# Performance work log

Measured on AMD Instinct MI355X. Metric: run time of the kernel, lower is better.

## Reference

```python
import jax, jax.numpy as jnp
import numpy as np

N, T, H, D = 512, 256, 512, 9  # batch, decode steps, hidden, feature dim


def setup_inputs() -> dict:
    key = jax.random.key(0)
    ks = jax.random.split(key, 4)
    s = 1.0 / np.sqrt(H)
    return {
        "x": jax.random.normal(ks[0], (N, T + 1, D), dtype=jnp.float32),
        "W_ih": jax.random.normal(ks[1], (4 * H, D), dtype=jnp.float32) * s,
        "W_hh": jax.random.normal(ks[2], (4 * H, H), dtype=jnp.float32) * s,
        "b_ih": jnp.zeros((4 * H,), dtype=jnp.float32),
        "b_hh": jnp.zeros((4 * H,), dtype=jnp.float32),
        "fc_W": jax.random.normal(ks[3], (D, H), dtype=jnp.float32) * s,
        "fc_b": jnp.zeros((D,), dtype=jnp.float32),
        "h0": jnp.zeros((1, H), dtype=jnp.float32),
        "c0": jnp.zeros((1, H), dtype=jnp.float32),
    }


def _lstm_cell(x_proj, h, c, W_hh, b_hh):
    # x_proj = x @ W_ih.T + b_ih, precomputed. PyTorch LSTMCell gate order: i, f, g, o
    gates = x_proj + h @ W_hh.T + b_hh
    i, f, g, o = jnp.split(gates, 4, axis=-1)
    c_new = jax.nn.sigmoid(f) * c + jax.nn.sigmoid(i) * jnp.tanh(g)
    h_new = jax.nn.sigmoid(o) * jnp.tanh(c_new)
    return h_new, c_new


def reference(x, W_ih, W_hh, b_ih, b_hh, fc_W, fc_b, h0, c0):
    n = x.shape[0]
    h = jnp.broadcast_to(h0, (n, h0.shape[1]))
    c = jnp.broadcast_to(c0, (n, c0.shape[1]))

    # Encode phase: consume all T+1 input steps (precompute input projections in one GEMM)
    x_proj = jnp.einsum('ntd,gd->tng', x, W_ih) + b_ih  # [T+1, N, 4H]

    def enc_step(carry, xp):
        h, c = carry
        h, c = _lstm_cell(xp, h, c, W_hh, b_hh)
        return (h, c), None

    (h, c), _ = jax.lax.scan(enc_step, (h, c), x_proj)

    # Decode phase: T steps with zero input (input projection reduces to b_ih)
    zero_proj = jnp.broadcast_to(b_ih, (n, b_ih.shape[0]))

    def dec_step(carry, _):
        h, c = carry
        h, c = _lstm_cell(zero_proj, h, c, W_hh, b_hh)
        out = jax.nn.sigmoid(h @ fc_W.T + fc_b)  # [N, D]
        return (h, c), out

    n_dec = x.shape[1] - 1
    _, outs = jax.lax.scan(dec_step, (h, c), None, length=n_dec)  # [T, N, D]
    return jnp.transpose(outs, (1, 0, 2))  # [N, T, D]
```

## Files before the change

kernel.cpp:

```cpp
#include <hip/hip_runtime.h>


#define TT 256
#define HH 512
#define DD 9
#define TP1 257
#define NSTEP 513
#define THREADS 512
#define NWG 256
#define NCL 8
#define WPC 32

#define WF_HI_B 0u
#define WF_LO_B 2097152u
#define HFRAG_B 4194304u
#define U32_B   8388608u

#define L_ST    0
#define L_EX    16384
#define L_HNEW  20480
#define L_WIH   21520
#define L_MISC  22160
#define L_TOT   22164

typedef short s8v __attribute__((ext_vector_type(8)));
typedef float f4v __attribute__((ext_vector_type(4)));
typedef int   i4v __attribute__((ext_vector_type(4)));

__device__ __forceinline__ float sigmoidf_(float v){ return 1.0f/(1.0f+__expf(-v)); }
__device__ __forceinline__ float tanhf_(float v){ return 1.0f - 2.0f/(__expf(2.0f*v)+1.0f); }
__device__ __forceinline__ unsigned short bf16hi_rne(float f){
    unsigned u = __float_as_uint(f);
    return (unsigned short)((u + 0x7fffu + ((u>>16)&1u)) >> 16);
}
#define B2F_LO(u) __uint_as_float(((unsigned)(u))<<16)
#define B2F_HI(u) __uint_as_float(((unsigned)(u)) & 0xffff0000u)

__device__ __forceinline__ void ld16i(i4v& d, const char* p){
    asm volatile("global_load_dwordx4 %0, %1, off sc0" : "=v"(d) : "v"(p));
}
__device__ __forceinline__ void wait_vm0_mem(){
    asm volatile("s_waitcnt vmcnt(0)" ::: "memory");
}
__device__ __forceinline__ void wait_vm0_4i(i4v& a0,i4v& a1,i4v& a2,i4v& a3){
    asm volatile("s_waitcnt vmcnt(0)"
                 : "+v"(a0),"+v"(a1),"+v"(a2),"+v"(a3) :: "memory");
}
__device__ __forceinline__ void lgkm0_bar(){
    asm volatile("s_waitcnt lgkmcnt(0)" ::: "memory");
    __builtin_amdgcn_s_barrier();
}

__global__ void rnn_init_kernel(const float* __restrict__ W_hh,
                                const float* __restrict__ h0,
                                char* __restrict__ wsb) {
    int idx = blockIdx.x * blockDim.x + threadIdx.x;
    {
        int i  = idx & 7;
        int l  = (idx >> 3) & 63;
        int kt = (idx >> 9) & 15;
        int rb = (idx >> 13) & 3;
        int wl = idx >> 15;
        int mm = l & 15, gg = l >> 4;
        int gt = mm & 3, lu = mm >> 2;
        int grow = gt * 512 + wl * 16 + rb * 4 + lu;
        int k = kt * 32 + gg * 8 + i;
        float v = W_hh[grow * 512 + k];
        unsigned short hi = bf16hi_rne(v);
        float fh = __uint_as_float(((unsigned)hi) << 16);
        unsigned short lo = bf16hi_rne(v - fh);
        ((unsigned short*)(wsb + WF_HI_B))[idx] = hi;
        ((unsigned short*)(wsb + WF_LO_B))[idx] = lo;
    }
    if (idx < 262144) {
        int i   = idx & 7;
        int gg  = (idx >> 9) & 3;
        int kt  = (idx >> 11) & 15;
        int cl  = idx >> 15;
        int rem = idx & 32767;
        int j = kt * 32 + gg * 8 + i;
        ((unsigned short*)(wsb + HFRAG_B + (unsigned)cl * 65536u))[rem] = bf16hi_rne(h0[j]);
    }
    if (idx < 2048) ((unsigned int*)(wsb + U32_B))[idx] = 0u;
}

__global__ __attribute__((amdgpu_waves_per_eu(2, 2))) __launch_bounds__(THREADS)
void rnn_persist_kernel(const float* __restrict__ x,
                        const float* __restrict__ W_ih,
                        const float* __restrict__ b_ih,
                        const float* __restrict__ b_hh,
                        const float* __restrict__ fc_W,
                        const float* __restrict__ fc_b,
                        const float* __restrict__ c0,
                        char* __restrict__ wsb,
                        float* __restrict__ out) {
    __shared__ float smem[L_TOT];
    char* ldsst = (char*)smem;

    const int wg  = blockIdx.x;
    const int cl  = wg & 7;
    const int wl  = wg >> 3;
    const int nb0 = cl * 64;
    const int tid = threadIdx.x;
    const int lane = tid & 63;
    const int wid  = tid >> 6;
    const int rb   = wid & 3;
    const int kh   = wid >> 2;
    const int m    = lane & 15;
    const int g    = lane >> 4;
    const int gu   = wl * 16 + rb * 4 + g;
    const int c0i  = kh * 32 + m;

    unsigned int* flags = (unsigned int*)(wsb + U32_B);
    unsigned int* ctr   = (unsigned int*)(wsb + U32_B + 3072);
    unsigned int* xccb  = (unsigned int*)(wsb + U32_B + 4096);

    for (int i2 = tid; i2 < 16 * 36; i2 += THREADS) {
        int u = i2 / 36; int r2 = i2 - u * 36; int gt = r2 / 9; int d = r2 - gt * 9;
        smem[L_WIH + u * 40 + gt * 9 + d] = W_ih[(gt * 512 + wl * 16 + u) * DD + d];
    }

    const float bias0 = b_ih[gu]        + b_hh[gu];
    const float bias1 = b_ih[512 + gu]  + b_hh[512 + gu];
    const float bias2 = b_ih[1024 + gu] + b_hh[1024 + gu];
    const float bias3 = b_ih[1536 + gu] + b_hh[1536 + gu];
    float creg0 = c0[gu], creg1 = c0[gu];

    s8v wAh[8], wAl[8];
    {
        const char* base = wsb + (unsigned)(((wl*4 + rb)*16 + kh*8)*64 + lane)*16u;
#pragma unroll
        for (int j = 0; j < 8; ++j) {
            wAh[j] = *(const s8v*)(base + WF_HI_B + j*1024);
            wAl[j] = *(const s8v*)(base + WF_LO_B + j*1024);
        }
    }

    if (tid == 0) {
        unsigned xcc;
        asm volatile("s_getreg_b32 %0, hwreg(HW_REG_XCC_ID, 0, 32)" : "=s"(xcc));
        __hip_atomic_store(xccb + wg, xcc + 1u, __ATOMIC_RELAXED, __HIP_MEMORY_SCOPE_AGENT);
        __hip_atomic_fetch_add(ctr, 1u, __ATOMIC_RELEASE, __HIP_MEMORY_SCOPE_AGENT);
        while (__hip_atomic_load(ctr, __ATOMIC_RELAXED, __HIP_MEMORY_SCOPE_AGENT) < NWG)
            __builtin_amdgcn_s_sleep(8);
    }
    __syncthreads();
    {
        unsigned v = (tid < WPC)
            ? __hip_atomic_load(xccb + cl + 8 * tid, __ATOMIC_RELAXED,
                                __HIP_MEMORY_SCOPE_AGENT) : 0u;
        unsigned v0 = __shfl(v, 0, 64);
        bool ok = (tid >= WPC) || (v != 0u && v == v0);
        unsigned long long mk = __ballot(ok);
        if (tid == 0) smem[L_MISC] = (mk == ~0ull) ? 1.0f : 0.0f;
    }
    __syncthreads();
    const bool fast = (smem[L_MISC] != 0.0f);

    const int fg = tid >> 4, fl = tid & 15;

    for (int s = 0; s < NSTEP; ++s) {
        const int par = s & 1;
        const char* hsrc = wsb + HFRAG_B + (unsigned)(par*8 + cl) * 65536u;
        unsigned int* flg = flags + cl * 32;
        const bool dec = (s >= TP1 + 1);
        const bool enc = (s < TP1);

        float xv0[DD], xv1[DD];
        if (enc) {
            const float* xp0 = x + (size_t)(nb0 + c0i) * (TP1 * DD) + s * DD;
            const float* xp1 = x + (size_t)(nb0 + c0i + 16) * (TP1 * DD) + s * DD;
#pragma unroll
            for (int d = 0; d < DD; ++d) { xv0[d] = xp0[d]; xv1[d] = xp1[d]; }
        }

        if (s > 0) {
            if (tid < WPC) {
                for (;;) {
                    unsigned v = __hip_atomic_load(flg + tid, __ATOMIC_RELAXED,
                                                   __HIP_MEMORY_SCOPE_AGENT);
                    if (__all((int)(v >= (unsigned)s))) break;
                    __builtin_amdgcn_s_sleep(2);
                }
            }
            __syncthreads();
            if (fast) __builtin_amdgcn_fence(__ATOMIC_ACQUIRE, "workgroup");
            else      __builtin_amdgcn_fence(__ATOMIC_ACQUIRE, "agent");
        }

        i4v hb[8];
#pragma unroll
        for (int c = 0; c < 8; ++c)
            ld16i(hb[c], hsrc + c*8192 + tid*16);

        wait_vm0_mem();
#pragma unroll
        for (int c = 0; c < 8; ++c)
            *(i4v*)(ldsst + c*8192 + tid*16) = hb[c];
        i4v qa0, qa1, qa2, qa3;
        if (dec) {
            const int bselL = (fg < 2 * DD) ? (fg / DD) : 0;
            const int blL = wl * 2 + bselL;
            const char* hp = hsrc + fl*4096 + blL*16;
            ld16i(qa0, hp);          ld16i(qa1, hp + 1024);
            ld16i(qa2, hp + 2048);   ld16i(qa3, hp + 3072);
        }
        lgkm0_bar();

        f4v a0 = {0,0,0,0}, a1 = {0,0,0,0}, a2 = {0,0,0,0}, a3 = {0,0,0,0};
        {
            const char* base = ldsst + kh*32768;
#pragma unroll
            for (int j = 0; j < 8; ++j) {
                const char* bb = base + j*4096 + g*1024 + m*16;
                s8v bh0 = *(const s8v*)(bb);
                s8v bh1 = *(const s8v*)(bb + 256);
                s8v bh2 = *(const s8v*)(bb + 512);
                s8v bh3 = *(const s8v*)(bb + 768);
                a0 = __builtin_amdgcn_mfma_f32_16x16x32_bf16(wAh[j], bh0, a0, 0,0,0);
                a1 = __builtin_amdgcn_mfma_f32_16x16x32_bf16(wAh[j], bh1, a1, 0,0,0);
                a2 = __builtin_amdgcn_mfma_f32_16x16x32_bf16(wAh[j], bh2, a2, 0,0,0);
                a3 = __builtin_amdgcn_mfma_f32_16x16x32_bf16(wAh[j], bh3, a3, 0,0,0);
                a0 = __builtin_amdgcn_mfma_f32_16x16x32_bf16(wAl[j], bh0, a0, 0,0,0);
                a1 = __builtin_amdgcn_mfma_f32_16x16x32_bf16(wAl[j], bh1, a1, 0,0,0);
                a2 = __builtin_amdgcn_mfma_f32_16x16x32_bf16(wAl[j], bh2, a2, 0,0,0);
                a3 = __builtin_amdgcn_mfma_f32_16x16x32_bf16(wAl[j], bh3, a3, 0,0,0);
            }
            float* pe = smem + L_EX + ((rb*2 + kh)*64 + lane)*8;
            if (kh == 0) { *(f4v*)(pe) = a2; *(f4v*)(pe + 4) = a3; }
            else         { *(f4v*)(pe) = a0; *(f4v*)(pe + 4) = a1; }
        }
        lgkm0_bar();

        {
            const float* px = smem + L_EX + ((rb*2 + (kh^1))*64 + lane)*8;
            f4v r0 = *(const f4v*)(px);
            f4v r1 = *(const f4v*)(px + 4);
            f4v ka, kb;
            if (kh == 0) { ka = a0 + r0; kb = a1 + r1; }
            else         { ka = a2 + r0; kb = a3 + r1; }

            float s00=0,s01=0,s02=0,s03=0, s10=0,s11=0,s12=0,s13=0;
            if (enc) {
                const float* wb2 = smem + L_WIH + (rb*4 + g) * 40;
#pragma unroll
                for (int r2 = 0; r2 < 9; ++r2) {
                    f4v w4 = *(const f4v*)(wb2 + r2*4);
#pragma unroll
                    for (int e = 0; e < 4; ++e) {
                        const int fl2 = r2*4 + e;
                        const int gt = fl2 / 9, d = fl2 - gt*9;
                        const float w = w4[e];
                        const float p0 = xv0[d] * w, p1 = xv1[d] * w;
                        if (gt == 0) { s00 += p0; s10 += p1; }
                        else if (gt == 1) { s01 += p0; s11 += p1; }
                        else if (gt == 2) { s02 += p0; s12 += p1; }
                        else { s03 += p0; s13 += p1; }
                    }
                }
            }
            {
                float vi = ka.x + bias0 + s00, vf = ka.y + bias1 + s01;
                float vg = ka.z + bias2 + s02, vo = ka.w + bias3 + s03;
                float cn = sigmoidf_(vf) * creg0 + sigmoidf_(vi) * tanhf_(vg);
                creg0 = cn;
                smem[L_HNEW + (rb*4 + g) * 65 + c0i] = sigmoidf_(vo) * tanhf_(cn);
            }
            {
                float vi = kb.x + bias0 + s10, vf = kb.y + bias1 + s11;
                float vg = kb.z + bias2 + s12, vo = kb.w + bias3 + s13;
                float cn = sigmoidf_(vf) * creg1 + sigmoidf_(vi) * tanhf_(vg);
                creg1 = cn;
                smem[L_HNEW + (rb*4 + g) * 65 + c0i + 16] = sigmoidf_(vo) * tanhf_(cn);
            }
        }
        lgkm0_bar();

        if (tid < 128) {
            const int col = tid & 63, jblk = (tid >> 6) & 1;
            const int jb = wl * 2 + jblk;
            const int kt = jb >> 2, gg = jb & 3;
            s8v v;
#pragma unroll
            for (int i = 0; i < 8; ++i)
                v[i] = (short)bf16hi_rne(smem[L_HNEW + (jblk * 8 + i) * 65 + col]);
            char* dst = wsb + HFRAG_B + (unsigned)((par^1)*8 + cl)*65536u
                        + (unsigned)(kt*4096 + gg*1024 + col*16);
            *(s8v*)dst = v;
        }
        wait_vm0_mem();
        __syncthreads();

        if (tid == 0) {
            if (fast) {
                __hip_atomic_store(flg + wl, (unsigned)(s + 1),
                                   __ATOMIC_RELAXED, __HIP_MEMORY_SCOPE_AGENT);
            } else {
                __builtin_amdgcn_fence(__ATOMIC_RELEASE, "agent");
                __hip_atomic_store(flg + wl, (unsigned)(s + 1),
                                   __ATOMIC_RELEASE, __HIP_MEMORY_SCOPE_AGENT);
            }
        }

        if (dec && fg < 2 * DD) {
            const int bsel = fg / DD, d = fg - bsel * DD;
            const int bl = wl * 2 + bsel;
            const f4v* wf = (const f4v*)(fc_W + d * HH + fl * 32);
            wait_vm0_4i(qa0, qa1, qa2, qa3);
            float acc = 0.f;
            acc += B2F_LO(qa0.x)*wf[0].x + B2F_HI(qa0.x)*wf[0].y
                 + B2F_LO(qa0.y)*wf[0].z + B2F_HI(qa0.y)*wf[0].w
                 + B2F_LO(qa0.z)*wf[1].x + B2F_HI(qa0.z)*wf[1].y
                 + B2F_LO(qa0.w)*wf[1].z + B2F_HI(qa0.w)*wf[1].w;
            acc += B2F_LO(qa1.x)*wf[2].x + B2F_HI(qa1.x)*wf[2].y
                 + B2F_LO(qa1.y)*wf[2].z + B2F_HI(qa1.y)*wf[2].w
                 + B2F_LO(qa1.z)*wf[3].x + B2F_HI(qa1.z)*wf[3].y
                 + B2F_LO(qa1.w)*wf[3].z + B2F_HI(qa1.w)*wf[3].w;
            acc += B2F_LO(qa2.x)*wf[4].x + B2F_HI(qa2.x)*wf[4].y
                 + B2F_LO(qa2.y)*wf[4].z + B2F_HI(qa2.y)*wf[4].w
                 + B2F_LO(qa2.z)*wf[5].x + B2F_HI(qa2.z)*wf[5].y
                 + B2F_LO(qa2.w)*wf[5].z + B2F_HI(qa2.w)*wf[5].w;
            acc += B2F_LO(qa3.x)*wf[6].x + B2F_HI(qa3.x)*wf[6].y
                 + B2F_LO(qa3.y)*wf[6].z + B2F_HI(qa3.y)*wf[6].w
                 + B2F_LO(qa3.z)*wf[7].x + B2F_HI(qa3.z)*wf[7].y
                 + B2F_LO(qa3.w)*wf[7].z + B2F_HI(qa3.w)*wf[7].w;
            acc += __shfl_down(acc, 8, 16);
            acc += __shfl_down(acc, 4, 16);
            acc += __shfl_down(acc, 2, 16);
            acc += __shfl_down(acc, 1, 16);
            if (fl == 0)
                out[(size_t)(nb0 + bl) * (TT * DD) + (s - (TP1 + 1)) * DD + d] =
                    1.0f / (1.0f + __expf(-(acc + fc_b[d])));
        }
    }

    {
        if (tid < WPC) {
            for (;;) {
                unsigned v = __hip_atomic_load(flags + cl * 32 + tid,
                                               __ATOMIC_RELAXED, __HIP_MEMORY_SCOPE_AGENT);
                if (__all((int)(v >= (unsigned)NSTEP))) break;
                __builtin_amdgcn_s_sleep(2);
            }
        }
        __syncthreads();
        if (fast) __builtin_amdgcn_fence(__ATOMIC_ACQUIRE, "workgroup");
        else      __builtin_amdgcn_fence(__ATOMIC_ACQUIRE, "agent");

        if (fg < 2 * DD) {
            const int bsel = fg / DD, d = fg - bsel * DD;
            const int bl = wl * 2 + bsel;
            const char* hp = wsb + HFRAG_B + (unsigned)((NSTEP & 1)*8 + cl)*65536u
                             + (unsigned)(fl*4096 + bl*16);
            i4v qa0, qa1, qa2, qa3;
            ld16i(qa0, hp);          ld16i(qa1, hp + 1024);
            ld16i(qa2, hp + 2048);   ld16i(qa3, hp + 3072);
            const f4v* wf = (const f4v*)(fc_W + d * HH + fl * 32);
            wait_vm0_4i(qa0, qa1, qa2, qa3);
            float acc = 0.f;
            acc += B2F_LO(qa0.x)*wf[0].x + B2F_HI(qa0.x)*wf[0].y
                 + B2F_LO(qa0.y)*wf[0].z + B2F_HI(qa0.y)*wf[0].w
                 + B2F_LO(qa0.z)*wf[1].x + B2F_HI(qa0.z)*wf[1].y
                 + B2F_LO(qa0.w)*wf[1].z + B2F_HI(qa0.w)*wf[1].w;
            acc += B2F_LO(qa1.x)*wf[2].x + B2F_HI(qa1.x)*wf[2].y
                 + B2F_LO(qa1.y)*wf[2].z + B2F_HI(qa1.y)*wf[2].w
                 + B2F_LO(qa1.z)*wf[3].x + B2F_HI(qa1.z)*wf[3].y
                 + B2F_LO(qa1.w)*wf[3].z + B2F_HI(qa1.w)*wf[3].w;
            acc += B2F_LO(qa2.x)*wf[4].x + B2F_HI(qa2.x)*wf[4].y
                 + B2F_LO(qa2.y)*wf[4].z + B2F_HI(qa2.y)*wf[4].w
                 + B2F_LO(qa2.z)*wf[5].x + B2F_HI(qa2.z)*wf[5].y
                 + B2F_LO(qa2.w)*wf[5].z + B2F_HI(qa2.w)*wf[5].w;
            acc += B2F_LO(qa3.x)*wf[6].x + B2F_HI(qa3.x)*wf[6].y
                 + B2F_LO(qa3.y)*wf[6].z + B2F_HI(qa3.y)*wf[6].w
                 + B2F_LO(qa3.z)*wf[7].x + B2F_HI(qa3.z)*wf[7].y
                 + B2F_LO(qa3.w)*wf[7].z + B2F_HI(qa3.w)*wf[7].w;
            acc += __shfl_down(acc, 8, 16);
            acc += __shfl_down(acc, 4, 16);
            acc += __shfl_down(acc, 2, 16);
            acc += __shfl_down(acc, 1, 16);
            if (fl == 0)
                out[(size_t)(nb0 + bl) * (TT * DD) + 255 * DD + d] =
                    1.0f / (1.0f + __expf(-(acc + fc_b[d])));
        }
    }
}

extern "C" void kernel_launch(void* const* d_in, const int* in_sizes, int n_in,
                              void* d_out, int out_size, void* d_ws, size_t ws_size,
                              hipStream_t stream) {
    (void)in_sizes; (void)n_in; (void)out_size; (void)ws_size;
    const float* x    = (const float*)d_in[0];
    const float* W_ih = (const float*)d_in[1];
    const float* W_hh = (const float*)d_in[2];
    const float* b_ih = (const float*)d_in[3];
    const float* b_hh = (const float*)d_in[4];
    const float* fc_W = (const float*)d_in[5];
    const float* fc_b = (const float*)d_in[6];
    const float* h0   = (const float*)d_in[7];
    const float* c0   = (const float*)d_in[8];
    float* out = (float*)d_out;
    char*  wsb = (char*)d_ws;

    hipLaunchKernelGGL(rnn_init_kernel, dim3(4096), dim3(256), 0, stream,
                       W_hh, h0, wsb);
    hipLaunchKernelGGL(rnn_persist_kernel, dim3(NWG), dim3(THREADS), 0, stream,
                       x, W_ih, b_ih, b_hh, fc_W, fc_b, c0, wsb, out);
}
```

Before: 2.299 ms.

## Repartition LSTM work into 16 batch clusters with full-K per wave

Changes the grid decomposition from 8 batch clusters of 64 rows with 32 workgroups each to 16 clusters of 32 rows with 16 workgroups each. Each wave now owns the full K=512 reduction for its hidden units, which removes the split-K partial-sum exchange through LDS and one barrier per step. Each workgroup now covers 32 hidden units instead of 16, so it holds twice as many W_hh fragments in registers. The per-step h broadcast per workgroup halves, and each flag barrier waits on 16 peers instead of 32. The cost is more register pressure and more MFMA work per wave on the serial critical path.

```diff
diff --git a/kernel.cpp b/kernel.cpp
--- a/kernel.cpp
+++ b/kernel.cpp
@@ -8,8 +8,8 @@
 #define NSTEP 513
 #define THREADS 512
 #define NWG 256
-#define NCL 8
-#define WPC 32
+#define NCL 16
+#define WPC 16
 
 #define WF_HI_B 0u
 #define WF_LO_B 2097152u
@@ -17,11 +17,10 @@
 #define U32_B   8388608u
 
 #define L_ST    0
-#define L_EX    16384
-#define L_HNEW  20480
-#define L_WIH   21520
-#define L_MISC  22160
-#define L_TOT   22164
+#define L_HNEW  8192
+#define L_WIH   9248
+#define L_MISC  10528
+#define L_TOT   10532
 
 typedef short s8v __attribute__((ext_vector_type(8)));
 typedef float f4v __attribute__((ext_vector_type(4)));
@@ -56,15 +55,15 @@
                                 char* __restrict__ wsb) {
     int idx = blockIdx.x * blockDim.x + threadIdx.x;
     {
-        int i  = idx & 7;
-        int l  = (idx >> 3) & 63;
-        int kt = (idx >> 9) & 15;
-        int rb = (idx >> 13) & 3;
-        int wl = idx >> 15;
-        int mm = l & 15, gg = l >> 4;
+        int i    = idx & 7;
+        int lane = (idx >> 3) & 63;
+        int kt   = (idx >> 9) & 15;
+        int rb   = (idx >> 13) & 7;
+        int wl   = idx >> 16;
+        int mm = lane & 15, g = lane >> 4;
         int gt = mm & 3, lu = mm >> 2;
-        int grow = gt * 512 + wl * 16 + rb * 4 + lu;
-        int k = kt * 32 + gg * 8 + i;
+        int grow = gt * 512 + wl * 32 + rb * 4 + lu;
+        int k = kt * 32 + g * 8 + i;
         float v = W_hh[grow * 512 + k];
         unsigned short hi = bf16hi_rne(v);
         float fh = __uint_as_float(((unsigned)hi) << 16);
@@ -74,12 +73,12 @@
     }
     if (idx < 262144) {
         int i   = idx & 7;
-        int gg  = (idx >> 9) & 3;
-        int kt  = (idx >> 11) & 15;
-        int cl  = idx >> 15;
-        int rem = idx & 32767;
+        int gg  = (idx >> 8) & 3;
+        int kt  = (idx >> 10) & 15;
+        int cl  = idx >> 14;
+        int rem = idx & 16383;
         int j = kt * 32 + gg * 8 + i;
-        ((unsigned short*)(wsb + HFRAG_B + (unsigned)cl * 65536u))[rem] = bf16hi_rne(h0[j]);
+        ((unsigned short*)(wsb + HFRAG_B + (unsigned)cl * 32768u))[rem] = bf16hi_rne(h0[j]);
     }
     if (idx < 2048) ((unsigned int*)(wsb + U32_B))[idx] = 0u;
 }
@@ -98,26 +97,24 @@
     char* ldsst = (char*)smem;
 
     const int wg  = blockIdx.x;
-    const int cl  = wg & 7;
-    const int wl  = wg >> 3;
-    const int nb0 = cl * 64;
+    const int cl  = wg & 15;
+    const int wl  = wg >> 4;
+    const int nb0 = cl * 32;
     const int tid = threadIdx.x;
     const int lane = tid & 63;
-    const int wid  = tid >> 6;
-    const int rb   = wid & 3;
-    const int kh   = wid >> 2;
+    const int rb   = tid >> 6;
     const int m    = lane & 15;
     const int g    = lane >> 4;
-    const int gu   = wl * 16 + rb * 4 + g;
-    const int c0i  = kh * 32 + m;
+    const int gu   = wl * 32 + rb * 4 + g;
+    const int uu   = rb * 4 + g;
 
     unsigned int* flags = (unsigned int*)(wsb + U32_B);
     unsigned int* ctr   = (unsigned int*)(wsb + U32_B + 3072);
     unsigned int* xccb  = (unsigned int*)(wsb + U32_B + 4096);
 
-    for (int i2 = tid; i2 < 16 * 36; i2 += THREADS) {
+    for (int i2 = tid; i2 < 32 * 36; i2 += THREADS) {
         int u = i2 / 36; int r2 = i2 - u * 36; int gt = r2 / 9; int d = r2 - gt * 9;
-        smem[L_WIH + u * 40 + gt * 9 + d] = W_ih[(gt * 512 + wl * 16 + u) * DD + d];
+        smem[L_WIH + u * 40 + gt * 9 + d] = W_ih[(gt * 512 + wl * 32 + u) * DD + d];
     }
 
     const float bias0 = b_ih[gu]        + b_hh[gu];
@@ -126,11 +123,11 @@
     const float bias3 = b_ih[1536 + gu] + b_hh[1536 + gu];
     float creg0 = c0[gu], creg1 = c0[gu];
 
-    s8v wAh[8], wAl[8];
+    s8v wAh[16], wAl[16];
     {
-        const char* base = wsb + (unsigned)(((wl*4 + rb)*16 + kh*8)*64 + lane)*16u;
-#pragma unroll
-        for (int j = 0; j < 8; ++j) {
+        const char* base = wsb + (unsigned)(((wl*8 + rb)*16)*64 + lane)*16u;
+#pragma unroll
+        for (int j = 0; j < 16; ++j) {
             wAh[j] = *(const s8v*)(base + WF_HI_B + j*1024);
             wAl[j] = *(const s8v*)(base + WF_LO_B + j*1024);
         }
@@ -147,7 +144,7 @@
     __syncthreads();
     {
         unsigned v = (tid < WPC)
-            ? __hip_atomic_load(xccb + cl + 8 * tid, __ATOMIC_RELAXED,
+            ? __hip_atomic_load(xccb + cl + 16 * tid, __ATOMIC_RELAXED,
                                 __HIP_MEMORY_SCOPE_AGENT) : 0u;
         unsigned v0 = __shfl(v, 0, 64);
         bool ok = (tid >= WPC) || (v != 0u && v == v0);
@@ -161,15 +158,15 @@
 
     for (int s = 0; s < NSTEP; ++s) {
         const int par = s & 1;
-        const char* hsrc = wsb + HFRAG_B + (unsigned)(par*8 + cl) * 65536u;
-        unsigned int* flg = flags + cl * 32;
+        const char* hsrc = wsb + HFRAG_B + (unsigned)(par*16 + cl) * 32768u;
+        unsigned int* flg = flags + cl * 16;
         const bool dec = (s >= TP1 + 1);
         const bool enc = (s < TP1);
 
         float xv0[DD], xv1[DD];
         if (enc) {
-            const float* xp0 = x + (size_t)(nb0 + c0i) * (TP1 * DD) + s * DD;
-            const float* xp1 = x + (size_t)(nb0 + c0i + 16) * (TP1 * DD) + s * DD;
+            const float* xp0 = x + (size_t)(nb0 + m) * (TP1 * DD) + s * DD;
+            const float* xp1 = x + (size_t)(nb0 + m + 16) * (TP1 * DD) + s * DD;
 #pragma unroll
             for (int d = 0; d < DD; ++d) { xv0[d] = xp0[d]; xv1[d] = xp1[d]; }
         }
@@ -188,61 +185,41 @@
             else      __builtin_amdgcn_fence(__ATOMIC_ACQUIRE, "agent");
         }
 
-        i4v hb[8];
-#pragma unroll
-        for (int c = 0; c < 8; ++c)
+        i4v hb[4];
+#pragma unroll
+        for (int c = 0; c < 4; ++c)
             ld16i(hb[c], hsrc + c*8192 + tid*16);
 
         wait_vm0_mem();
 #pragma unroll
-        for (int c = 0; c < 8; ++c)
+        for (int c = 0; c < 4; ++c)
             *(i4v*)(ldsst + c*8192 + tid*16) = hb[c];
         i4v qa0, qa1, qa2, qa3;
         if (dec) {
             const int bselL = (fg < 2 * DD) ? (fg / DD) : 0;
             const int blL = wl * 2 + bselL;
-            const char* hp = hsrc + fl*4096 + blL*16;
-            ld16i(qa0, hp);          ld16i(qa1, hp + 1024);
-            ld16i(qa2, hp + 2048);   ld16i(qa3, hp + 3072);
+            const char* hp = hsrc + fl*2048 + blL*16;
+            ld16i(qa0, hp);          ld16i(qa1, hp + 512);
+            ld16i(qa2, hp + 1024);   ld16i(qa3, hp + 1536);
         }
         lgkm0_bar();
 
-        f4v a0 = {0,0,0,0}, a1 = {0,0,0,0}, a2 = {0,0,0,0}, a3 = {0,0,0,0};
+        f4v a0 = {0,0,0,0}, a1 = {0,0,0,0};
+#pragma unroll
+        for (int j = 0; j < 16; ++j) {
+            const char* bb = ldsst + j*2048 + g*512 + m*16;
+            s8v bh0 = *(const s8v*)(bb);
+            s8v bh1 = *(const s8v*)(bb + 256);
+            a0 = __builtin_amdgcn_mfma_f32_16x16x32_bf16(wAh[j], bh0, a0, 0,0,0);
+            a1 = __builtin_amdgcn_mfma_f32_16x16x32_bf16(wAh[j], bh1, a1, 0,0,0);
+            a0 = __builtin_amdgcn_mfma_f32_16x16x32_bf16(wAl[j], bh0, a0, 0,0,0);
+            a1 = __builtin_amdgcn_mfma_f32_16x16x32_bf16(wAl[j], bh1, a1, 0,0,0);
+        }
+
         {
-            const char* base = ldsst + kh*32768;
-#pragma unroll
-            for (int j = 0; j < 8; ++j) {
-                const char* bb = base + j*4096 + g*1024 + m*16;
-                s8v bh0 = *(const s8v*)(bb);
-                s8v bh1 = *(const s8v*)(bb + 256);
-                s8v bh2 = *(const s8v*)(bb + 512);
-                s8v bh3 = *(const s8v*)(bb + 768);
-                a0 = __builtin_amdgcn_mfma_f32_16x16x32_bf16(wAh[j], bh0, a0, 0,0,0);
-                a1 = __builtin_amdgcn_mfma_f32_16x16x32_bf16(wAh[j], bh1, a1, 0,0,0);
-                a2 = __builtin_amdgcn_mfma_f32_16x16x32_bf16(wAh[j], bh2, a2, 0,0,0);
-                a3 = __builtin_amdgcn_mfma_f32_16x16x32_bf16(wAh[j], bh3, a3, 0,0,0);
-                a0 = __builtin_amdgcn_mfma_f32_16x16x32_bf16(wAl[j], bh0, a0, 0,0,0);
-                a1 = __builtin_amdgcn_mfma_f32_16x16x32_bf16(wAl[j], bh1, a1, 0,0,0);
-                a2 = __builtin_amdgcn_mfma_f32_16x16x32_bf16(wAl[j], bh2, a2, 0,0,0);
-                a3 = __builtin_amdgcn_mfma_f32_16x16x32_bf16(wAl[j], bh3, a3, 0,0,0);
-            }
-            float* pe = smem + L_EX + ((rb*2 + kh)*64 + lane)*8;
-            if (kh == 0) { *(f4v*)(pe) = a2; *(f4v*)(pe + 4) = a3; }
-            else         { *(f4v*)(pe) = a0; *(f4v*)(pe + 4) = a1; }
-        }
-        lgkm0_bar();
-
-        {
-            const float* px = smem + L_EX + ((rb*2 + (kh^1))*64 + lane)*8;
-            f4v r0 = *(const f4v*)(px);
-            f4v r1 = *(const f4v*)(px + 4);
-            f4v ka, kb;
-            if (kh == 0) { ka = a0 + r0; kb = a1 + r1; }
-            else         { ka = a2 + r0; kb = a3 + r1; }
-
             float s00=0,s01=0,s02=0,s03=0, s10=0,s11=0,s12=0,s13=0;
             if (enc) {
-                const float* wb2 = smem + L_WIH + (rb*4 + g) * 40;
+                const float* wb2 = smem + L_WIH + uu * 40;
 #pragma unroll
                 for (int r2 = 0; r2 < 9; ++r2) {
                     f4v w4 = *(const f4v*)(wb2 + r2*4);
@@ -260,32 +237,30 @@
                 }
             }
             {
-                float vi = ka.x + bias0 + s00, vf = ka.y + bias1 + s01;
-                float vg = ka.z + bias2 + s02, vo = ka.w + bias3 + s03;
+                float vi = a0.x + bias0 + s00, vf = a0.y + bias1 + s01;
+                float vg = a0.z + bias2 + s02, vo = a0.w + bias3 + s03;
                 float cn = sigmoidf_(vf) * creg0 + sigmoidf_(vi) * tanhf_(vg);
                 creg0 = cn;
-                smem[L_HNEW + (rb*4 + g) * 65 + c0i] = sigmoidf_(vo) * tanhf_(cn);
+                smem[L_HNEW + uu * 33 + m] = sigmoidf_(vo) * tanhf_(cn);
             }
             {
-                float vi = kb.x + bias0 + s10, vf = kb.y + bias1 + s11;
-                float vg = kb.z + bias2 + s12, vo = kb.w + bias3 + s13;
+                float vi = a1.x + bias0 + s10, vf = a1.y + bias1 + s11;
+                float vg = a1.z + bias2 + s12, vo = a1.w + bias3 + s13;
                 float cn = sigmoidf_(vf) * creg1 + sigmoidf_(vi) * tanhf_(vg);
                 creg1 = cn;
-                smem[L_HNEW + (rb*4 + g) * 65 + c0i + 16] = sigmoidf_(vo) * tanhf_(cn);
+                smem[L_HNEW + uu * 33 + m + 16] = sigmoidf_(vo) * tanhf_(cn);
             }
         }
         lgkm0_bar();
 
         if (tid < 128) {
-            const int col = tid & 63, jblk = (tid >> 6) & 1;
-            const int jb = wl * 2 + jblk;
-            const int kt = jb >> 2, gg = jb & 3;
+            const int col = tid & 31, gg = tid >> 5;
             s8v v;
 #pragma unroll
             for (int i = 0; i < 8; ++i)
-                v[i] = (short)bf16hi_rne(smem[L_HNEW + (jblk * 8 + i) * 65 + col]);
-            char* dst = wsb + HFRAG_B + (unsigned)((par^1)*8 + cl)*65536u
-                        + (unsigned)(kt*4096 + gg*1024 + col*16);
+                v[i] = (short)bf16hi_rne(smem[L_HNEW + (gg * 8 + i) * 33 + col]);
+            char* dst = wsb + HFRAG_B + (unsigned)((par^1)*16 + cl)*32768u
+                        + (unsigned)(wl*2048 + gg*512 + col*16);
             *(s8v*)dst = v;
         }
         wait_vm0_mem();
@@ -337,7 +312,7 @@
     {
         if (tid < WPC) {
             for (;;) {
-                unsigned v = __hip_atomic_load(flags + cl * 32 + tid,
+                unsigned v = __hip_atomic_load(flags + cl * 16 + tid,
                                                __ATOMIC_RELAXED, __HIP_MEMORY_SCOPE_AGENT);
                 if (__all((int)(v >= (unsigned)NSTEP))) break;
                 __builtin_amdgcn_s_sleep(2);
@@ -350,11 +325,11 @@
         if (fg < 2 * DD) {
             const int bsel = fg / DD, d = fg - bsel * DD;
             const int bl = wl * 2 + bsel;
-            const char* hp = wsb + HFRAG_B + (unsigned)((NSTEP & 1)*8 + cl)*65536u
-                             + (unsigned)(fl*4096 + bl*16);
+            const char* hp = wsb + HFRAG_B + (unsigned)((NSTEP & 1)*16 + cl)*32768u
+                             + (unsigned)(fl*2048 + bl*16);
             i4v qa0, qa1, qa2, qa3;
-            ld16i(qa0, hp);          ld16i(qa1, hp + 1024);
-            ld16i(qa2, hp + 2048);   ld16i(qa3, hp + 3072);
+            ld16i(qa0, hp);          ld16i(qa1, hp + 512);
+            ld16i(qa2, hp + 1024);   ld16i(qa3, hp + 1536);
             const f4v* wf = (const f4v*)(fc_W + d * HH + fl * 32);
             wait_vm0_4i(qa0, qa1, qa2, qa3);
             float acc = 0.f;
```

After: 2.102 ms. 8.5% less time.
